# Kernel tuning notes

Hardware: AMD Instinct MI355X
Metric: run time of the kernel (lower is better)

Reference implementation:

```python
import jax, jax.numpy as jnp
import numpy as np

B, S, I, H = 32, 4096, 512, 512
NEG_INF = -1e18


def setup_inputs() -> dict:
    key = jax.random.key(0)
    ks = jax.random.split(key, 8)
    query = jax.random.normal(ks[0], (B, I), dtype=jnp.float32)
    kv = jax.random.normal(ks[1], (B, S, I), dtype=jnp.float32)
    mask = jax.random.randint(ks[2], (B, S), 0, 2).astype(jnp.bool_)
    # q_proj: Linear(I, H) with bias
    lim_q = 1.0 / np.sqrt(I)
    Wq = jax.random.uniform(ks[3], (H, I), minval=-lim_q, maxval=lim_q, dtype=jnp.float32)
    bq = jax.random.uniform(ks[4], (H,), minval=-lim_q, maxval=lim_q, dtype=jnp.float32)
    # k_proj: Conv1d(I, H, kernel_size=1) == pointwise linear; weight squeezed to [H, I]
    Wk = jax.random.uniform(ks[5], (H, I), minval=-lim_q, maxval=lim_q, dtype=jnp.float32)
    bk = jax.random.uniform(ks[6], (H,), minval=-lim_q, maxval=lim_q, dtype=jnp.float32)
    # out: Linear(H, 1, bias=False), init uniform(-1, 1); squeeze to [H]
    Wout = jax.random.uniform(ks[7], (H,), minval=-1.0, maxval=1.0, dtype=jnp.float32)
    return {"query": query, "key": kv, "mask": mask,
            "Wq": Wq, "bq": bq, "Wk": Wk, "bk": bk, "Wout": Wout}


def reference(query, key, mask, Wq, bq, Wk, bk, Wout):
    # q: [B, H]
    q = query @ Wq.T + bq
    # k: conv1d kernel-size-1 == per-position linear -> [B, S, H]
    k = jnp.einsum('bsi,hi->bsh', key, Wk) + bk
    # additive attention score: out((q + k)) -> [B, S]
    scores = jnp.einsum('bsh,h->bs', q[:, None, :] + k, Wout)
    attn_weight = jnp.where(mask, jnp.float32(NEG_INF), scores)
    attn_prob = jax.nn.softmax(attn_weight, axis=-1)
    # bmm(k^T-form [B, H, S], prob [B, S, 1]) -> [B, H]
    attn = jnp.einsum('bsh,bs->bh', k, attn_prob)
    return attn, attn_weight
```

## Files before the change

kernel.cpp:

```cpp
#include <hip/hip_runtime.h>
#include <math.h>

constexpr int B = 32, S = 4096, I = 512, H = 512;
constexpr int CH = 128;
constexpr int NCH = S / CH;
constexpr float NEGV = -1e18f;

constexpr size_t WS_WKD   = 0;
constexpr size_t WS_WQD   = 512;
constexpr size_t WS_CC    = 1024;
constexpr size_t WS_PARTS = 2048;

__global__ __launch_bounds__(256) void prep_kernel(
    const float* __restrict__ Wq, const float* __restrict__ bq,
    const float* __restrict__ Wk, const float* __restrict__ bk,
    const float* __restrict__ Wout, float* __restrict__ ws) {
  __shared__ float sh[256];
  int blk = blockIdx.x;
  int t = threadIdx.x, wv = t >> 6, ln = t & 63;

  if (blk < 16) {
    bool isQ = blk >= 8;
    const float* W = isQ ? Wq : Wk;
    float* out = ws + (isQ ? WS_WQD : WS_WKD);
    int j = (blk & 7) * 64 + ln;
    int h0 = wv * 128;
    float p = 0.f;
    for (int hb = 0; hb < 128; hb += 16) {
      float v[16];
      #pragma unroll
      for (int r = 0; r < 16; ++r)
        v[r] = W[(size_t)(h0 + hb + r) * I + j];
      #pragma unroll
      for (int r = 0; r < 16; ++r)
        p = fmaf(v[r], Wout[h0 + hb + r], p);
    }
    sh[wv * 64 + ln] = p;
    __syncthreads();
    if (t < 64) out[(blk & 7) * 64 + t] = sh[t] + sh[64 + t] + sh[128 + t] + sh[192 + t];
  } else {
    float p = 0.f;
    for (int h = t; h < H; h += 256) p = fmaf(bq[h] + bk[h], Wout[h], p);
    sh[t] = p;
    __syncthreads();
    for (int o = 128; o; o >>= 1) {
      if (t < o) sh[t] += sh[t + o];
      __syncthreads();
    }
    if (t == 0) ws[WS_CC] = sh[0];
  }
}

__global__ __launch_bounds__(256, 4) void main_kernel(
    const float* __restrict__ query,
    const float* __restrict__ key, const int* __restrict__ mask,
    float* __restrict__ ws, float* __restrict__ attn_w) {
  const float* wkd = ws + WS_WKD;
  const float* wqd = ws + WS_WQD;
  float* parts = ws + WS_PARTS;

  int b = blockIdx.x, cidx = blockIdx.y;
  int t = threadIdx.x, wv = t >> 6, ln = t & 63;

  float offb;
  {
    const float* qb = query + (size_t)b * I;
    float p = qb[ln] * wqd[ln];
    #pragma unroll
    for (int k = 1; k < 8; ++k)
      p = fmaf(qb[ln + 64 * k], wqd[ln + 64 * k], p);
    #pragma unroll
    for (int o = 32; o; o >>= 1) p += __shfl_xor(p, o, 64);
    offb = p + ws[WS_CC];
  }

  const float* kb = key + ((size_t)b * S + (size_t)cidx * CH) * I;
  const int* mrow = mask + (size_t)b * S + cidx * CH;
  float* awrow = attn_w + (size_t)b * S + cidx * CH;

  float4 wA = *(const float4*)(wkd + ln * 4);
  float4 wB = *(const float4*)(wkd + 256 + ln * 4);

  float m = -INFINITY, l = 0.f;
  float4 cA = {0.f, 0.f, 0.f, 0.f}, cB = {0.f, 0.f, 0.f, 0.f};

  constexpr int NIT = CH / 8;
  const float* lanep = kb + (size_t)(wv * 2) * I + ln * 4;
  constexpr int ROWSTEP = 8 * I;

  float4 uA0 = *(const float4*)(lanep);
  float4 uB0 = *(const float4*)(lanep + 256);
  float4 uA1 = *(const float4*)(lanep + 512);
  float4 uB1 = *(const float4*)(lanep + 768);
  float4 vA0 = *(const float4*)(lanep + ROWSTEP);
  float4 vB0 = *(const float4*)(lanep + ROWSTEP + 256);
  float4 vA1 = *(const float4*)(lanep + ROWSTEP + 512);
  float4 vB1 = *(const float4*)(lanep + ROWSTEP + 768);

  #pragma unroll 2
  for (int it = 0; it < NIT; ++it) {
    int s = wv * 2 + it * 8;
    int itn = (it + 2 < NIT) ? it + 2 : it;
    const float* kn = lanep + (size_t)itn * ROWSTEP;
    float4 nA0 = *(const float4*)(kn);
    float4 nB0 = *(const float4*)(kn + 256);
    float4 nA1 = *(const float4*)(kn + 512);
    float4 nB1 = *(const float4*)(kn + 768);

    float d0 = uA0.x * wA.x, d1 = uA1.x * wA.x;
    d0 = fmaf(uA0.y, wA.y, d0); d1 = fmaf(uA1.y, wA.y, d1);
    d0 = fmaf(uA0.z, wA.z, d0); d1 = fmaf(uA1.z, wA.z, d1);
    d0 = fmaf(uA0.w, wA.w, d0); d1 = fmaf(uA1.w, wA.w, d1);
    d0 = fmaf(uB0.x, wB.x, d0); d1 = fmaf(uB1.x, wB.x, d1);
    d0 = fmaf(uB0.y, wB.y, d0); d1 = fmaf(uB1.y, wB.y, d1);
    d0 = fmaf(uB0.z, wB.z, d0); d1 = fmaf(uB1.z, wB.z, d1);
    d0 = fmaf(uB0.w, wB.w, d0); d1 = fmaf(uB1.w, wB.w, d1);
    #pragma unroll
    for (int o = 32; o; o >>= 1) {
      d0 += __shfl_xor(d0, o, 64);
      d1 += __shfl_xor(d1, o, 64);
    }

    int2 mm = *(const int2*)(mrow + s);
    float s0 = mm.x ? NEGV : (offb + d0);
    float s1 = mm.y ? NEGV : (offb + d1);
    if (ln == 0) *(float2*)(awrow + s) = float2{s0, s1};

    float mx = fmaxf(s0, s1);
    if (mx > m) {
      float sc = __expf(m - mx);
      l *= sc;
      cA.x *= sc; cA.y *= sc; cA.z *= sc; cA.w *= sc;
      cB.x *= sc; cB.y *= sc; cB.z *= sc; cB.w *= sc;
      m = mx;
    }
    float e0 = __expf(s0 - m);
    float e1 = __expf(s1 - m);
    l += e0 + e1;
    cA.x = fmaf(e0, uA0.x, fmaf(e1, uA1.x, cA.x));
    cA.y = fmaf(e0, uA0.y, fmaf(e1, uA1.y, cA.y));
    cA.z = fmaf(e0, uA0.z, fmaf(e1, uA1.z, cA.z));
    cA.w = fmaf(e0, uA0.w, fmaf(e1, uA1.w, cA.w));
    cB.x = fmaf(e0, uB0.x, fmaf(e1, uB1.x, cB.x));
    cB.y = fmaf(e0, uB0.y, fmaf(e1, uB1.y, cB.y));
    cB.z = fmaf(e0, uB0.z, fmaf(e1, uB1.z, cB.z));
    cB.w = fmaf(e0, uB0.w, fmaf(e1, uB1.w, cB.w));

    uA0 = vA0; uB0 = vB0; uA1 = vA1; uB1 = vB1;
    vA0 = nA0; vB0 = nB0; vA1 = nA1; vB1 = nB1;
  }

  __shared__ float shm[4], shl[4];
  __shared__ float shc[4][512];
  if (ln == 0) { shm[wv] = m; shl[wv] = l; }
  *(float4*)&shc[wv][ln * 4] = cA;
  *(float4*)&shc[wv][256 + ln * 4] = cB;
  __syncthreads();

  float mb = fmaxf(fmaxf(shm[0], shm[1]), fmaxf(shm[2], shm[3]));
  float ew0 = __expf(shm[0] - mb), ew1 = __expf(shm[1] - mb);
  float ew2 = __expf(shm[2] - mb), ew3 = __expf(shm[3] - mb);
  float* slot = parts + ((size_t)b * NCH + cidx) * 514;
  if (t == 0) {
    slot[0] = mb;
    slot[1] = shl[0] * ew0 + shl[1] * ew1 + shl[2] * ew2 + shl[3] * ew3;
  }
  for (int i = t; i < I; i += 256) {
    float acc = shc[0][i] * ew0;
    acc = fmaf(shc[1][i], ew1, acc);
    acc = fmaf(shc[2][i], ew2, acc);
    acc = fmaf(shc[3][i], ew3, acc);
    slot[2 + i] = acc;
  }
}

__global__ __launch_bounds__(256) void finish_kernel(
    const float* __restrict__ Wk, const float* __restrict__ bk,
    float* __restrict__ ws, float* __restrict__ attn) {
  const float* parts = ws + WS_PARTS;
  int b = blockIdx.x, hq = blockIdx.y, t = threadIdx.x;

  __shared__ float eld[NCH];
  __shared__ __align__(16) float ctx[I];
  const float* pb = parts + (size_t)b * NCH * 514;

  float m = -INFINITY;
  #pragma unroll 8
  for (int p = 0; p < NCH; ++p) m = fmaxf(m, pb[p * 514]);
  float l = 0.f;
  #pragma unroll 8
  for (int p = 0; p < NCH; ++p) l = fmaf(pb[p * 514 + 1], __expf(pb[p * 514] - m), l);
  float invl = 1.f / l;
  if (t < NCH) eld[t] = __expf(pb[t * 514] - m) * invl;
  __syncthreads();

  {
    float a0 = 0.f, a1 = 0.f;
    #pragma unroll 8
    for (int p = 0; p < NCH; ++p) {
      float e = eld[p];
      a0 = fmaf(pb[p * 514 + 2 + t], e, a0);
      a1 = fmaf(pb[p * 514 + 258 + t], e, a1);
    }
    ctx[t] = a0;
    ctx[t + 256] = a1;
  }
  __syncthreads();

  int h = hq * 64 + (t >> 2), q = t & 3;
  const float4* wrow = (const float4*)(Wk + (size_t)h * I);
  const float4* cvec = (const float4*)ctx;
  float a0 = 0.f, a1 = 0.f;
  #pragma unroll 8
  for (int c = 0; c < 32; c += 2) {
    float4 w0 = wrow[q + 4 * c];
    float4 w1 = wrow[q + 4 * (c + 1)];
    float4 x0 = cvec[q + 4 * c];
    float4 x1 = cvec[q + 4 * (c + 1)];
    a0 = fmaf(w0.x, x0.x, fmaf(w0.y, x0.y, fmaf(w0.z, x0.z, fmaf(w0.w, x0.w, a0))));
    a1 = fmaf(w1.x, x1.x, fmaf(w1.y, x1.y, fmaf(w1.z, x1.z, fmaf(w1.w, x1.w, a1))));
  }
  float a = a0 + a1;
  a += __shfl_xor(a, 1, 64);
  a += __shfl_xor(a, 2, 64);
  if (q == 0) attn[(size_t)b * H + h] = a + bk[h];
}

extern "C" void kernel_launch(void* const* d_in, const int* in_sizes, int n_in,
                              void* d_out, int out_size, void* d_ws, size_t ws_size,
                              hipStream_t stream) {
  const float* query = (const float*)d_in[0];
  const float* key   = (const float*)d_in[1];
  const int*   mask  = (const int*)d_in[2];
  const float* Wq    = (const float*)d_in[3];
  const float* bq    = (const float*)d_in[4];
  const float* Wk    = (const float*)d_in[5];
  const float* bk    = (const float*)d_in[6];
  const float* Wout  = (const float*)d_in[7];

  float* attn   = (float*)d_out;
  float* attn_w = (float*)d_out + (size_t)B * H;
  float* ws     = (float*)d_ws;

  prep_kernel<<<17, 256, 0, stream>>>(Wq, bq, Wk, bk, Wout, ws);
  main_kernel<<<dim3(B, NCH), 256, 0, stream>>>(query, key, mask, ws, attn_w);
  finish_kernel<<<dim3(B, 8), 256, 0, stream>>>(Wk, bk, ws, attn);
}
```

Measured before the change: 70.22 us.

## Fuse finish kernel into main kernel via per-batch atomic arrival counter

Removes the separate finish kernel launch. Each main-kernel block bumps a per-batch atomic counter after writing its partial. The last NFIN arrivals per batch spin-wait until all chunks are done, then perform the softmax merge and the Wk projection for one 64-row slice, reusing shared memory. It also widens the prep kernel's weight-load batch from 16 to 32 rows. This saves a launch and the inter-kernel gap, but it relies on forward progress of the spinning blocks and adds atomic and fence overhead.

```diff
diff --git a/kernel.cpp b/kernel.cpp
--- a/kernel.cpp
+++ b/kernel.cpp
@@ -4,11 +4,13 @@
 constexpr int B = 32, S = 4096, I = 512, H = 512;
 constexpr int CH = 128;
 constexpr int NCH = S / CH;
+constexpr int NFIN = 8;
 constexpr float NEGV = -1e18f;
 
 constexpr size_t WS_WKD   = 0;
 constexpr size_t WS_WQD   = 512;
 constexpr size_t WS_CC    = 1024;
+constexpr size_t WS_CNT   = 1056;
 constexpr size_t WS_PARTS = 2048;
 
 __global__ __launch_bounds__(256) void prep_kernel(
@@ -26,19 +28,20 @@
     int j = (blk & 7) * 64 + ln;
     int h0 = wv * 128;
     float p = 0.f;
-    for (int hb = 0; hb < 128; hb += 16) {
-      float v[16];
+    for (int hb = 0; hb < 128; hb += 32) {
+      float v[32];
       #pragma unroll
-      for (int r = 0; r < 16; ++r)
+      for (int r = 0; r < 32; ++r)
         v[r] = W[(size_t)(h0 + hb + r) * I + j];
       #pragma unroll
-      for (int r = 0; r < 16; ++r)
+      for (int r = 0; r < 32; ++r)
         p = fmaf(v[r], Wout[h0 + hb + r], p);
     }
     sh[wv * 64 + ln] = p;
     __syncthreads();
     if (t < 64) out[(blk & 7) * 64 + t] = sh[t] + sh[64 + t] + sh[128 + t] + sh[192 + t];
   } else {
+    if (t < B) ((int*)(ws + WS_CNT))[t] = 0;
     float p = 0.f;
     for (int h = t; h < H; h += 256) p = fmaf(bq[h] + bk[h], Wout[h], p);
     sh[t] = p;
@@ -54,7 +57,9 @@
 __global__ __launch_bounds__(256, 4) void main_kernel(
     const float* __restrict__ query,
     const float* __restrict__ key, const int* __restrict__ mask,
-    float* __restrict__ ws, float* __restrict__ attn_w) {
+    const float* __restrict__ Wk, const float* __restrict__ bk,
+    float* __restrict__ ws, float* __restrict__ attn_w,
+    float* __restrict__ attn) {
   const float* wkd = ws + WS_WKD;
   const float* wqd = ws + WS_WQD;
   float* parts = ws + WS_PARTS;
@@ -151,7 +156,7 @@
   }
 
   __shared__ float shm[4], shl[4];
-  __shared__ float shc[4][512];
+  __shared__ __align__(16) float shc[4][512];
   if (ln == 0) { shm[wv] = m; shl[wv] = l; }
   *(float4*)&shc[wv][ln * 4] = cA;
   *(float4*)&shc[wv][256 + ln * 4] = cB;
@@ -172,26 +177,38 @@
     acc = fmaf(shc[3][i], ew3, acc);
     slot[2 + i] = acc;
   }
-}
-
-__global__ __launch_bounds__(256) void finish_kernel(
-    const float* __restrict__ Wk, const float* __restrict__ bk,
-    float* __restrict__ ws, float* __restrict__ attn) {
-  const float* parts = ws + WS_PARTS;
-  int b = blockIdx.x, hq = blockIdx.y, t = threadIdx.x;
-
-  __shared__ float eld[NCH];
-  __shared__ __align__(16) float ctx[I];
+
+  __syncthreads();
+  __shared__ int svv;
+  int* cntb = (int*)(ws + WS_CNT) + b;
+  if (t == 0) {
+    __threadfence();
+    svv = atomicAdd(cntb, 1);
+  }
+  __syncthreads();
+  int v = svv;
+  if (v < NCH - NFIN) return;
+  int hq = v - (NCH - NFIN);
+
+  if (t == 0) {
+    while (__hip_atomic_load(cntb, __ATOMIC_ACQUIRE, __HIP_MEMORY_SCOPE_AGENT) < NCH)
+      __builtin_amdgcn_s_sleep(2);
+  }
+  __syncthreads();
+  __threadfence();
+
   const float* pb = parts + (size_t)b * NCH * 514;
-
-  float m = -INFINITY;
+  float* eld = &shc[0][0];
+  float* ctx = &shc[1][0];
+
+  float m2 = -INFINITY;
   #pragma unroll 8
-  for (int p = 0; p < NCH; ++p) m = fmaxf(m, pb[p * 514]);
-  float l = 0.f;
+  for (int p = 0; p < NCH; ++p) m2 = fmaxf(m2, pb[p * 514]);
+  float l2 = 0.f;
   #pragma unroll 8
-  for (int p = 0; p < NCH; ++p) l = fmaf(pb[p * 514 + 1], __expf(pb[p * 514] - m), l);
-  float invl = 1.f / l;
-  if (t < NCH) eld[t] = __expf(pb[t * 514] - m) * invl;
+  for (int p = 0; p < NCH; ++p) l2 = fmaf(pb[p * 514 + 1], __expf(pb[p * 514] - m2), l2);
+  float invl = 1.f / l2;
+  if (t < NCH) eld[t] = __expf(pb[t * 514] - m2) * invl;
   __syncthreads();
 
   {
@@ -243,6 +260,6 @@
   float* ws     = (float*)d_ws;
 
   prep_kernel<<<17, 256, 0, stream>>>(Wq, bq, Wk, bk, Wout, ws);
-  main_kernel<<<dim3(B, NCH), 256, 0, stream>>>(query, key, mask, ws, attn_w);
-  finish_kernel<<<dim3(B, 8), 256, 0, stream>>>(Wk, bk, ws, attn);
+  main_kernel<<<dim3(B, NCH), 256, 0, stream>>>(query, key, mask, Wk, bk,
+                                                ws, attn_w, attn);
 }
```

Result: slower. 139.6 us (+98.8%).
